# Optimization experiments

Hardware: AMD Instinct MI355X
Metric: run time of the kernel (lower is better)

Reference implementation:

```python
import jax, jax.numpy as jnp
import numpy as np
from jax import lax

B, T = 32, 20
H, E, A, V = 256, 512, 256, 10000
GH, GW, D = 32, 32, 256          # info spatial grid and channel dim
P = GH * GW                      # num_pixels = 1024
IN_FLAT = P * D                  # 262144
REL = 128 * 128                  # 16384
LSTM_IN = E + D + H              # input to gate linears (x = [word, att_feat], then cat h)


def setup_inputs() -> dict:
    key = jax.random.key(0)
    ks = iter(jax.random.split(key, 40))
    def W(shape, scale=0.05):
        return jax.random.normal(next(ks), shape, jnp.float32) * scale
    inp = {}
    inp["info"] = jax.random.normal(next(ks), (B, GH, GW, D), jnp.float32)
    inp["relation"] = jax.random.normal(next(ks), (B, 128, 128), jnp.float32)
    inp["captions"] = jax.random.randint(next(ks), (B, T), 0, V)
    lens = jax.random.randint(next(ks), (B, 1), 5, T + 1).at[0, 0].set(T)
    inp["captions_lens"] = lens
    # embedding + attention
    inp["emb"] = W((V, E), 0.1)
    inp["W_enc"] = W((D, A)); inp["b_enc"] = jnp.zeros((A,), jnp.float32)
    inp["W_dec"] = W((H, A)); inp["b_dec"] = jnp.zeros((A,), jnp.float32)
    inp["W_full"] = W((A,));  inp["b_full"] = jnp.zeros((), jnp.float32)
    # MSLSTM cell (5 gate linears + mlp)
    for g in ("i", "f", "o", "g1", "g2"):
        inp[f"W_{g}"] = W((LSTM_IN, H)); inp[f"b_{g}"] = jnp.zeros((H,), jnp.float32)
    inp["W_mlp"] = W((2 * H, H)); inp["b_mlp"] = jnp.zeros((H,), jnp.float32)
    # f_beta, fc, init-state linears
    inp["W_beta"] = W((H, D)); inp["b_beta"] = jnp.zeros((D,), jnp.float32)
    inp["W_fc"] = W((H, V), 0.1); inp["b_fc"] = jnp.zeros((V,), jnp.float32)
    inp["W_ih"] = W((IN_FLAT, H), 0.005); inp["b_ih"] = jnp.zeros((H,), jnp.float32)
    inp["W_ic"] = W((IN_FLAT, H), 0.005); inp["b_ic"] = jnp.zeros((H,), jnp.float32)
    inp["W_iC"] = W((REL, H), 0.01);      inp["b_iC"] = jnp.zeros((H,), jnp.float32)
    return inp


def reference(info, relation, captions, captions_lens, emb,
              W_enc, b_enc, W_dec, b_dec, W_full, b_full,
              W_i, b_i, W_f, b_f, W_o, b_o, W_g1, b_g1, W_g2, b_g2,
              W_mlp, b_mlp, W_beta, b_beta, W_fc, b_fc,
              W_ih, b_ih, W_ic, b_ic, W_iC, b_iC):
    Bsz = captions.shape[0]
    info_f = info.reshape(Bsz, P, D)
    rel_f = relation.reshape(Bsz, REL)
    lens = captions_lens[:, 0]
    order = jnp.argsort(-lens)                      # sort descending by length
    lens = lens[order]
    caps = captions[order]
    info_f = info_f[order]
    rel_f = rel_f[order]
    sent_len = lens - 1
    Tm = captions.shape[1] - 1                      # static: max len forced to T in setup

    words = emb[caps]                               # (B, T, E)
    flat = info_f.reshape(Bsz, -1)                  # (B, P*D)
    h = flat @ W_ih + b_ih
    c = flat @ W_ic + b_ic
    C = rel_f @ W_iC + b_iC
    att1 = info_f @ W_enc + b_enc                   # (B, P, A) -- invariant over t

    def step(carry, xs):
        h, c, C = carry
        word, t = xs                                # word: (B, E)
        att2 = h @ W_dec + b_dec                    # (B, A)
        e = jax.nn.relu(att1 + att2[:, None, :]) @ W_full + b_full   # (B, P)
        alpha = jax.nn.softmax(e, axis=1)
        awf = jnp.einsum('bpd,bp->bd', info_f, alpha)                # (B, D)
        # note: gate=sigmoid(f_beta(h)) is computed in torch but its product is unused
        x = jnp.concatenate([word, awf, h], axis=1)  # cat([x, h]) with x=[word, awf]
        i = jax.nn.sigmoid(x @ W_i + b_i)
        f = jax.nn.sigmoid(x @ W_f + b_f)
        o = jax.nn.sigmoid(x @ W_o + b_o)
        g1 = jnp.tanh(x @ W_g1 + b_g1)
        g2 = jnp.tanh(x @ W_g2 + b_g2)
        new_c = f * c + i * g1
        new_C = f * C + i * g2
        new_h = o * jnp.tanh(jnp.concatenate([new_c, new_C], axis=1) @ W_mlp + b_mlp)
        pred = new_h @ W_fc + b_fc                  # dropout in eval mode = identity
        mask = (sent_len > t)[:, None].astype(pred.dtype)
        return (new_h, new_c, new_C), (pred * mask, alpha * mask)

    words_t = jnp.swapaxes(words[:, :Tm], 0, 1)     # (Tm, B, E)
    (_, (preds, alphas)) = lax.scan(step, (h, c, C), (words_t, jnp.arange(Tm)))
    predictions = jnp.swapaxes(preds, 0, 1)         # (B, Tm, V)
    alphas = jnp.swapaxes(alphas, 0, 1)             # (B, Tm, P)
    return predictions, alphas, order
```

## Files before the change

### kernel.cpp

```cpp
#include <hip/hip_runtime.h>
#include <math.h>

#define Bz 32
#define Tz 20
#define TMz 19
#define Vz 10000
#define INFLAT 262144
#define RELSZ 16384
#define NBLK 512

#define WS_PH     0
#define WS_PC     4194304
#define WS_ATT1H  0
#define WS_INFOH  4194304
#define WS_EXPE   8388608
#define WS_ZSUM   8421376
#define WS_AWF    8421888
#define WS_GSP    8430080
#define WS_HST    8593920
#define WS_CST0   8602112
#define WS_CSTB0  8610304
#define WS_CST1   8618496
#define WS_CSTB1  8626688
#define WS_AT2P   8634880
#define WS_INTS   8700416
#define WS_PCHC   8701440

__device__ __forceinline__ float sigm(float x) { return 1.0f / (1.0f + expf(-x)); }

__device__ __forceinline__ unsigned short f2bf(float f) {
    unsigned int x = __float_as_uint(f);
    unsigned int r = (x + 0x7fffu + ((x >> 16) & 1u)) >> 16;
    return (unsigned short)r;
}
__device__ __forceinline__ float bfl(unsigned int u) { return __uint_as_float(u << 16); }
__device__ __forceinline__ float bfh(unsigned int u) { return __uint_as_float(u & 0xffff0000u); }

__device__ __forceinline__ float agload(const float* p) {
    return __hip_atomic_load(p, __ATOMIC_RELAXED, __HIP_MEMORY_SCOPE_AGENT);
}
__device__ __forceinline__ void agstore(float* p, float v) {
    __hip_atomic_store(p, v, __ATOMIC_RELAXED, __HIP_MEMORY_SCOPE_AGENT);
}
__device__ __forceinline__ int agloadi(const int* p) {
    return __hip_atomic_load(p, __ATOMIC_RELAXED, __HIP_MEMORY_SCOPE_AGENT);
}
__device__ __forceinline__ void agstorei(int* p, int v) {
    __hip_atomic_store(p, v, __ATOMIC_RELAXED, __HIP_MEMORY_SCOPE_AGENT);
}
__device__ __forceinline__ void agadd(float* p, float v) {
    __hip_atomic_fetch_add(p, v, __ATOMIC_RELAXED, __HIP_MEMORY_SCOPE_AGENT);
}

__device__ __forceinline__ void gl_lds16(const float* g, float* l) {
    __builtin_amdgcn_global_load_lds(
        (const __attribute__((address_space(1))) unsigned int*)g,
        (__attribute__((address_space(3))) unsigned int*)l,
        16, 0, 0);
}

__device__ __forceinline__ void gbar(int* slots, int* root, int gen) {
    asm volatile("s_waitcnt vmcnt(0)" ::: "memory");
    __syncthreads();
    if (blockIdx.x == 0) {
        int i0 = threadIdx.x, i1 = threadIdx.x + 256;
        if (i0 != 0) {
            while (agloadi(&slots[i0]) < gen) __builtin_amdgcn_s_sleep(1);
        }
        while (agloadi(&slots[i1]) < gen) __builtin_amdgcn_s_sleep(1);
        __syncthreads();
        if (threadIdx.x == 0) agstorei(root, gen);
    } else if (threadIdx.x == 0) {
        agstorei(&slots[blockIdx.x], gen);
        while (agloadi(root) < gen) __builtin_amdgcn_s_sleep(2);
    }
    __syncthreads();
    asm volatile("" ::: "memory");
}

__global__ void k_sort(const int* __restrict__ lens, float* __restrict__ out_order,
                       int* __restrict__ ord, int* __restrict__ sentlen, int* __restrict__ barmem) {
    if (threadIdx.x == 0 && blockIdx.x == 0) {
        for (int i = 0; i < 64 + NBLK; ++i) barmem[i] = 0;
        int l[Bz]; bool used[Bz];
        for (int b = 0; b < Bz; ++b) { l[b] = lens[b]; used[b] = false; }
        for (int i = 0; i < Bz; ++i) {
            int best = -1;
            for (int j = 0; j < Bz; ++j)
                if (!used[j] && (best < 0 || l[j] > l[best])) best = j;
            used[best] = true;
            ord[i] = best;
            sentlen[i] = l[best] - 1;
            out_order[i] = (float)best;
        }
    }
}

__global__ __launch_bounds__(256) void k_gemv2(const float* __restrict__ X, const int* __restrict__ ord,
                                               const float* __restrict__ W1, const float* __restrict__ W2,
                                               float* __restrict__ p1, float* __restrict__ p2) {
    __shared__ __align__(16) float wlds[8192];
    __shared__ __align__(16) float xsT[256 * 36];
    __shared__ int ords[32];
    int tid = threadIdx.x;
    int wv = tid >> 6, ln = tid & 63;
    size_t k0 = (size_t)blockIdx.x * 512;

    if (tid < 32) ords[tid] = ord[tid];
    __syncthreads();

    auto stage_xs = [&](int hh) {
        for (int idx = tid; idx < 2048; idx += 256) {
            int b = idx >> 6, kq = idx & 63;
            float4 v = *(const float4*)&X[(size_t)ords[b] * INFLAT + k0 + (size_t)hh * 256 + kq * 4];
            xsT[(kq * 4 + 0) * 36 + b] = v.x;
            xsT[(kq * 4 + 1) * 36 + b] = v.y;
            xsT[(kq * 4 + 2) * 36 + b] = v.z;
            xsT[(kq * 4 + 3) * 36 + b] = v.w;
        }
    };
    auto issue = [&](int n) {
        int slot = n & 1;
        size_t krow = k0 + (size_t)n * 8 + wv * 2;
        const float* g1 = W1 + krow * 256 + ln * 4;
        const float* g2 = W2 + krow * 256 + ln * 4;
        float* l1 = &wlds[slot * 4096 + (wv * 2) * 256 + ln * 4];
        float* l2 = &wlds[slot * 4096 + 2048 + (wv * 2) * 256 + ln * 4];
        gl_lds16(g1, l1);
        gl_lds16(g2, l2);
        gl_lds16(g1 + 256, l1 + 256);
        gl_lds16(g2 + 256, l2 + 256);
    };

    float ah[32], ac[32];
#pragma unroll
    for (int b = 0; b < 32; ++b) { ah[b] = 0.f; ac[b] = 0.f; }

    stage_xs(0);
    issue(0);

#pragma unroll 1
    for (int c = 0; c < 64; ++c) {
        if (c == 32) stage_xs(1);
        if (c + 1 < 64) {
            issue(c + 1);
            asm volatile("s_waitcnt vmcnt(4)" ::: "memory");
        } else {
            asm volatile("s_waitcnt vmcnt(0)" ::: "memory");
        }
        __syncthreads();
        int slot = c & 1;
        int xb0 = (c & 31) * 8;
#pragma unroll
        for (int kk = 0; kk < 8; ++kk) {
            float w1 = wlds[slot * 4096 + kk * 256 + tid];
            float w2 = wlds[slot * 4096 + 2048 + kk * 256 + tid];
            const float4* xr = (const float4*)&xsT[(xb0 + kk) * 36];
#pragma unroll
            for (int bq = 0; bq < 8; ++bq) {
                float4 x4 = xr[bq];
                ah[bq * 4 + 0] += x4.x * w1; ac[bq * 4 + 0] += x4.x * w2;
                ah[bq * 4 + 1] += x4.y * w1; ac[bq * 4 + 1] += x4.y * w2;
                ah[bq * 4 + 2] += x4.z * w1; ac[bq * 4 + 2] += x4.z * w2;
                ah[bq * 4 + 3] += x4.w * w1; ac[bq * 4 + 3] += x4.w * w2;
            }
        }
        __syncthreads();
    }
#pragma unroll
    for (int b = 0; b < 32; ++b) {
        size_t o = ((size_t)blockIdx.x * 32 + b) * 256 + tid;
        p1[o] = ah[b];
        p2[o] = ac[b];
    }
}

__global__ __launch_bounds__(256) void k_gemvC(const float* __restrict__ R, const int* __restrict__ ord,
                                               const float* __restrict__ W, float* __restrict__ p) {
    __shared__ float xs[32 * 128];
    __shared__ int ords[32];
    int tid = threadIdx.x, bx = blockIdx.x;
    if (tid < 32) ords[tid] = ord[tid];
    __syncthreads();
    int k0 = bx * 128;
    for (int idx = tid; idx < 32 * 128; idx += 256) {
        int b = idx >> 7, kk = idx & 127;
        xs[idx] = R[(size_t)ords[b] * RELSZ + k0 + kk];
    }
    __syncthreads();
    float acc[32];
#pragma unroll
    for (int b = 0; b < 32; ++b) acc[b] = 0.f;
    for (int kk = 0; kk < 128; ++kk) {
        float w = W[(size_t)(k0 + kk) * 256 + tid];
#pragma unroll
        for (int b = 0; b < 32; ++b) acc[b] += xs[b * 128 + kk] * w;
    }
#pragma unroll
    for (int b = 0; b < 32; ++b) p[((size_t)bx * 32 + b) * 256 + tid] = acc[b];
}

__global__ __launch_bounds__(256) void k_reduce3(const float* __restrict__ ph, const float* __restrict__ pc,
                                                 const float* __restrict__ pC,
                                                 const float* __restrict__ b_ih, const float* __restrict__ b_ic,
                                                 const float* __restrict__ b_iC,
                                                 float* __restrict__ hst, float* __restrict__ cst,
                                                 float* __restrict__ Cst) {
    int which = blockIdx.x >> 5, b = blockIdx.x & 31, j = threadIdx.x;
    if (which == 0) {
        float s0 = b_ih[j], s1 = 0.f, s2 = 0.f, s3 = 0.f;
        for (int c = 0; c < 512; c += 4) {
            s0 += ph[((size_t)((c + 0) * 32 + b)) * 256 + j];
            s1 += ph[((size_t)((c + 1) * 32 + b)) * 256 + j];
            s2 += ph[((size_t)((c + 2) * 32 + b)) * 256 + j];
            s3 += ph[((size_t)((c + 3) * 32 + b)) * 256 + j];
        }
        hst[b * 256 + j] = s0 + s1 + s2 + s3;
    } else if (which == 1) {
        float s0 = b_ic[j], s1 = 0.f, s2 = 0.f, s3 = 0.f;
        for (int c = 0; c < 512; c += 4) {
            s0 += pc[((size_t)((c + 0) * 32 + b)) * 256 + j];
            s1 += pc[((size_t)((c + 1) * 32 + b)) * 256 + j];
            s2 += pc[((size_t)((c + 2) * 32 + b)) * 256 + j];
            s3 += pc[((size_t)((c + 3) * 32 + b)) * 256 + j];
        }
        cst[b * 256 + j] = s0 + s1 + s2 + s3;
    } else {
        float s0 = b_iC[j], s1 = 0.f, s2 = 0.f, s3 = 0.f;
        for (int c = 0; c < 128; c += 4) {
            s0 += pC[((size_t)((c + 0) * 32 + b)) * 256 + j];
            s1 += pC[((size_t)((c + 1) * 32 + b)) * 256 + j];
            s2 += pC[((size_t)((c + 2) * 32 + b)) * 256 + j];
            s3 += pC[((size_t)((c + 3) * 32 + b)) * 256 + j];
        }
        Cst[b * 256 + j] = s0 + s1 + s2 + s3;
    }
}

__global__ __launch_bounds__(256) void k_init2(const float* __restrict__ hst, const float* __restrict__ W_dec,
                                               float* __restrict__ at2p, float* __restrict__ awf,
                                               float* __restrict__ zsum) {
    __shared__ __align__(16) float hs[8192];
    int tid = threadIdx.x;
    for (int i = blockIdx.x * 256 + tid; i < 8192; i += 1024) awf[i] = 0.f;
    if (blockIdx.x == 0 && tid < 32) zsum[tid] = 0.f;
    for (int i = tid; i < 2048; i += 256) ((float4*)hs)[i] = ((const float4*)hst)[i];
    __syncthreads();
    int col = blockIdx.x * 64 + (tid & 63), bg = tid >> 6;
    float acc[8] = {0.f,0.f,0.f,0.f,0.f,0.f,0.f,0.f};
    for (int k = 0; k < 256; ++k) {
        float w = W_dec[(size_t)k * 256 + col];
#pragma unroll
        for (int bi = 0; bi < 8; ++bi) acc[bi] += hs[(bg * 8 + bi) * 256 + k] * w;
    }
#pragma unroll
    for (int bi = 0; bi < 8; ++bi) {
        int b = bg * 8 + bi;
        at2p[((size_t)(b * 8 + 0)) * 256 + col] = acc[bi];
#pragma unroll
        for (int ct = 1; ct < 8; ++ct) at2p[((size_t)(b * 8 + ct)) * 256 + col] = 0.f;
    }
}

__global__ __launch_bounds__(256) void k_att1(const float* __restrict__ info, const int* __restrict__ ord,
                                              const float* __restrict__ W, const float* __restrict__ bias,
                                              unsigned short* __restrict__ att1h,
                                              unsigned short* __restrict__ infoh) {
    __shared__ __align__(16) float xsT[256 * 36];
    int tid = threadIdx.x;
    int r0 = blockIdx.x * 32;
    int b = r0 >> 10, p0 = r0 & 1023;
    const float* src = info + (size_t)ord[b] * INFLAT + (size_t)p0 * 256;
    for (int idx = tid; idx < 2048; idx += 256) {
        int r = idx >> 6, kq = idx & 63;
        float4 v = *(const float4*)&src[r * 256 + kq * 4];
        xsT[(kq * 4 + 0) * 36 + r] = v.x;
        xsT[(kq * 4 + 1) * 36 + r] = v.y;
        xsT[(kq * 4 + 2) * 36 + r] = v.z;
        xsT[(kq * 4 + 3) * 36 + r] = v.w;
    }
    __syncthreads();
#pragma unroll 4
    for (int r = 0; r < 32; ++r)
        infoh[(size_t)(r0 + r) * 256 + tid] = f2bf(xsT[tid * 36 + r]);
    float acc[32];
#pragma unroll
    for (int r = 0; r < 32; ++r) acc[r] = 0.f;
    for (int k = 0; k < 256; ++k) {
        float w = W[k * 256 + tid];
        const float4* xr = (const float4*)&xsT[k * 36];
#pragma unroll
        for (int rq = 0; rq < 8; ++rq) {
            float4 x4 = xr[rq];
            acc[rq * 4 + 0] += x4.x * w;
            acc[rq * 4 + 1] += x4.y * w;
            acc[rq * 4 + 2] += x4.z * w;
            acc[rq * 4 + 3] += x4.w * w;
        }
    }
    float bj = bias[tid];
#pragma unroll
    for (int r = 0; r < 32; ++r)
        att1h[(size_t)(r0 + r) * 256 + tid] = f2bf(acc[r] + bj);
}

struct KArgs {
    const float *info, *emb, *W_dec, *b_dec, *W_full, *b_full;
    const float *W_i, *W_f, *W_o, *W_g1, *W_g2;
    const float *b_i, *b_f, *b_o, *b_g1, *b_g2;
    const float *W_mlp, *b_mlp, *W_fc, *b_fc;
    const int *caps;
    const unsigned short *att1h, *infoh;
    float *expe, *zsum, *awf, *gsp, *hst, *cst0, *Cst0, *cst1, *Cst1, *at2p;
    const int *ord, *slp;
    int *root, *slots;
    float *out_pred, *out_alpha;
};

__device__ void pred_task2(const KArgs& a, unsigned short* hb, int tile, int tm1) {
    int tid = threadIdx.x;
    for (int i = tid; i < 8192; i += 256) hb[i] = f2bf(agload(&a.hst[i]));
    __syncthreads();
    int col = tile * 64 + (tid & 63), bg = tid >> 6;
    if (col >= Vz) return;
    float acc[8] = {0.f, 0.f, 0.f, 0.f, 0.f, 0.f, 0.f, 0.f};
    for (int jq = 0; jq < 64; ++jq) {
        float w0 = a.W_fc[(size_t)(jq * 4 + 0) * Vz + col];
        float w1 = a.W_fc[(size_t)(jq * 4 + 1) * Vz + col];
        float w2 = a.W_fc[(size_t)(jq * 4 + 2) * Vz + col];
        float w3 = a.W_fc[(size_t)(jq * 4 + 3) * Vz + col];
#pragma unroll
        for (int bi = 0; bi < 8; ++bi) {
            uint2 u = *(const uint2*)&hb[(bg * 8 + bi) * 256 + jq * 4];
            acc[bi] += bfl(u.x) * w0 + bfh(u.x) * w1 + bfl(u.y) * w2 + bfh(u.y) * w3;
        }
    }
    float bv = a.b_fc[col];
#pragma unroll
    for (int bi = 0; bi < 8; ++bi) {
        int b = bg * 8 + bi;
        float r = (a.slp[b] > tm1) ? (acc[bi] + bv) : 0.f;
        a.out_pred[((size_t)b * TMz + tm1) * Vz + col] = r;
    }
}

__global__ __launch_bounds__(256, 2) void k_steps(KArgs a) {
    __shared__ __align__(16) unsigned char smem[81920];
    unsigned char* attB = smem;
    unsigned char* infB = smem + 32768;
    float* F = (float*)(smem + 65536);
    unsigned short* S16 = (unsigned short*)(smem + 65536);

    int bid = blockIdx.x, tid = threadIdx.x;
    int b = bid >> 4, sub = bid & 15;
    int gen = 0;

    {
        const unsigned short* ag = a.att1h + (size_t)(b * 1024 + sub * 64) * 256;
        const unsigned short* ig = a.infoh + (size_t)(b * 1024 + sub * 64) * 256;
        for (int idx = tid; idx < 2048; idx += 256) {
            int r = idx >> 5, qc = idx & 31;
            uint4 v = *(const uint4*)(ag + (size_t)r * 256 + qc * 8);
            *(uint4*)(attB + r * 512 + ((qc ^ (r & 7)) << 4)) = v;
            uint4 w2 = *(const uint4*)(ig + (size_t)r * 256 + qc * 8);
            *(uint4*)(infB + idx * 16) = w2;
        }
    }
    __syncthreads();

    for (int t = 0; t < TMz; ++t) {
        {
            float v = a.b_dec[tid];
#pragma unroll
            for (int ct = 0; ct < 8; ++ct) v += agload(&a.at2p[((size_t)(b * 8 + ct)) * 256 + tid]);
            F[tid] = v;
            F[256 + tid] = a.W_full[tid];
            __syncthreads();
            int pl = tid & 63, kq = tid >> 6;
            float part = 0.f;
#pragma unroll
            for (int q = 0; q < 8; ++q) {
                int c = kq * 8 + q;
                uint4 u = *(const uint4*)(attB + pl * 512 + ((c ^ (pl & 7)) << 4));
                const float* A = F + kq * 64 + q * 8;
                const float* W = F + 256 + kq * 64 + q * 8;
                part += fmaxf(bfl(u.x) + A[0], 0.f) * W[0];
                part += fmaxf(bfh(u.x) + A[1], 0.f) * W[1];
                part += fmaxf(bfl(u.y) + A[2], 0.f) * W[2];
                part += fmaxf(bfh(u.y) + A[3], 0.f) * W[3];
                part += fmaxf(bfl(u.z) + A[4], 0.f) * W[4];
                part += fmaxf(bfh(u.z) + A[5], 0.f) * W[5];
                part += fmaxf(bfl(u.w) + A[6], 0.f) * W[6];
                part += fmaxf(bfh(u.w) + A[7], 0.f) * W[7];
            }
            F[512 + kq * 64 + pl] = part;
            __syncthreads();
            if (tid < 64) {
                float e = F[512 + tid] + F[576 + tid] + F[640 + tid] + F[704 + tid] + a.b_full[0];
                float ex = expf(e);
                agstore(&a.expe[b * 1024 + sub * 64 + tid], ex);
                F[768 + tid] = ex;
                float s = ex;
                s += __shfl_down(s, 32); s += __shfl_down(s, 16); s += __shfl_down(s, 8);
                s += __shfl_down(s, 4);  s += __shfl_down(s, 2);  s += __shfl_down(s, 1);
                if (tid == 0) agadd(&a.zsum[b], s);
            }
            __syncthreads();
            int gg = tid >> 7, c2 = tid & 127;
            const unsigned char* ib = infB + gg * 512 + c2 * 4;
            const float* ex = F + 768;
            float a0 = 0.f, a1 = 0.f;
#pragma unroll
            for (int i = 0; i < 32; ++i) {
                unsigned int u = *(const unsigned int*)(ib + i * 1024);
                float ev = ex[i * 2 + gg];
                a0 += ev * bfl(u);
                a1 += ev * bfh(u);
            }
            F[832 + gg * 256 + c2 * 2]     = a0;
            F[832 + gg * 256 + c2 * 2 + 1] = a1;
            __syncthreads();
            agadd(&a.awf[b * 256 + tid], F[832 + tid] + F[1088 + tid]);
        }
        gbar(a.slots, a.root, ++gen);

        if (bid < 80) {
            int g = bid / 16, s16 = bid % 16;
            int ct = s16 >> 2, kc = s16 & 3;
            const float* Wg = (g == 0) ? a.W_i : (g == 1) ? a.W_f : (g == 2) ? a.W_o : (g == 3) ? a.W_g1 : a.W_g2;
            for (int idx = tid; idx < 8192; idx += 256) {
                int b2 = idx >> 8, kk = idx & 255;
                float v;
                if (kc == 0) {
                    int cap = a.caps[a.ord[b2] * Tz + t];
                    v = a.emb[(size_t)cap * 512 + kk];
                } else if (kc == 1) {
                    int cap = a.caps[a.ord[b2] * Tz + t];
                    v = a.emb[(size_t)cap * 512 + 256 + kk];
                } else if (kc == 2) {
                    v = agload(&a.awf[b2 * 256 + kk]);
                } else {
                    v = agload(&a.hst[b2 * 256 + kk]);
                }
                S16[idx] = f2bf(v);
            }
            __syncthreads();
            int col = ct * 64 + (tid & 63), bg = tid >> 6;
            float acc[8] = {0.f,0.f,0.f,0.f,0.f,0.f,0.f,0.f};
            int wbase = kc * 256;
            for (int kk = 0; kk < 256; kk += 4) {
                float w0 = Wg[(size_t)(wbase + kk + 0) * 256 + col];
                float w1 = Wg[(size_t)(wbase + kk + 1) * 256 + col];
                float w2 = Wg[(size_t)(wbase + kk + 2) * 256 + col];
                float w3 = Wg[(size_t)(wbase + kk + 3) * 256 + col];
#pragma unroll
                for (int bi = 0; bi < 8; ++bi) {
                    uint2 u = *(const uint2*)&S16[(bg * 8 + bi) * 256 + kk];
                    acc[bi] += bfl(u.x) * w0 + bfh(u.x) * w1 + bfl(u.y) * w2 + bfh(u.y) * w3;
                }
            }
            if (kc == 2) {
#pragma unroll
                for (int bi = 0; bi < 8; ++bi) {
                    float Z = agload(&a.zsum[bg * 8 + bi]);
                    acc[bi] *= (1.0f / Z);
                }
            }
#pragma unroll
            for (int bi = 0; bi < 8; ++bi)
                agstore(&a.gsp[((size_t)((g * 4 + kc) * 32 + bg * 8 + bi)) * 256 + col], acc[bi]);
        } else if (bid < 237) {
            if (bid < 112) {
                int bb = bid - 80;
                float Z = agload(&a.zsum[bb]);
                float invZ = 1.0f / Z;
                float am = (a.slp[bb] > t) ? invZ : 0.f;
                float* oal = a.out_alpha + ((size_t)bb * TMz + t) * 1024;
                for (int p = tid; p < 1024; p += 256) oal[p] = agload(&a.expe[bb * 1024 + p]) * am;
            }
            if (t > 0) pred_task2(a, S16, bid - 80, t - 1);
        }
        gbar(a.slots, a.root, ++gen);

        if (bid < 256) {
            int bb = bid >> 3, ct = bid & 7;
            int j = tid;
            const float* csOld = (t & 1) ? a.cst1 : a.cst0;
            const float* CsOld = (t & 1) ? a.Cst1 : a.Cst0;
            float* csNew = (t & 1) ? a.cst0 : a.cst1;
            float* CsNew = (t & 1) ? a.Cst0 : a.Cst1;
            float gs[5];
#pragma unroll
            for (int g = 0; g < 5; ++g) {
                float s = 0.f;
#pragma unroll
                for (int kc = 0; kc < 4; ++kc)
                    s += agload(&a.gsp[((size_t)((g * 4 + kc) * 32 + bb)) * 256 + j]);
                gs[g] = s;
            }
            gs[0] += a.b_i[j]; gs[1] += a.b_f[j]; gs[2] += a.b_o[j];
            gs[3] += a.b_g1[j]; gs[4] += a.b_g2[j];
            float iv = sigm(gs[0]), fv = sigm(gs[1]), ov = sigm(gs[2]);
            float g1 = tanhf(gs[3]), g2 = tanhf(gs[4]);
            float nc = fv * agload(&csOld[bb * 256 + j]) + iv * g1;
            float nC = fv * agload(&CsOld[bb * 256 + j]) + iv * g2;
            if (ct == 0) {
                agstore(&csNew[bb * 256 + j], nc);
                agstore(&CsNew[bb * 256 + j], nC);
            }
            if (ct == 1 && tid == 0) agstore(&a.zsum[bb], 0.f);
            F[j] = nc;
            F[256 + j] = nC;
            F[512 + j] = ov;
            __syncthreads();
            int colL = tid & 31, kth = tid >> 5;
            int col = ct * 32 + colL;
            float part = 0.f;
            const float* wm = a.W_mlp + col;
            for (int i = 0; i < 64; ++i) {
                int k = kth * 64 + i;
                part += F[k] * wm[(size_t)k * 256];
            }
            F[768 + colL * 9 + kth] = part;
            __syncthreads();
            if (tid < 32) {
                int c2 = ct * 32 + tid;
                float m = a.b_mlp[c2];
#pragma unroll
                for (int kk = 0; kk < 8; ++kk) m += F[768 + tid * 9 + kk];
                float hv = F[512 + c2] * tanhf(m);
                agstore(&a.hst[bb * 256 + c2], hv);
                F[1056 + tid] = hv;
                agstore(&a.awf[bb * 256 + c2], 0.f);
            }
            __syncthreads();
            float acc = 0.f;
            const float* wd = a.W_dec + (size_t)(ct * 32) * 256 + tid;
#pragma unroll
            for (int kk = 0; kk < 32; ++kk) acc += F[1056 + kk] * wd[(size_t)kk * 256];
            agstore(&a.at2p[((size_t)(bb * 8 + ct)) * 256 + tid], acc);
        }
        gbar(a.slots, a.root, ++gen);
    }

    if (bid >= 80 && bid < 237) pred_task2(a, S16, bid - 80, TMz - 1);
}

extern "C" void kernel_launch(void* const* d_in, const int* in_sizes, int n_in,
                              void* d_out, int out_size, void* d_ws, size_t ws_size,
                              hipStream_t stream) {
    const float* info  = (const float*)d_in[0];
    const float* rel   = (const float*)d_in[1];
    const int*   caps  = (const int*)d_in[2];
    const int*   lens  = (const int*)d_in[3];
    const float* emb   = (const float*)d_in[4];
    const float* W_enc = (const float*)d_in[5];
    const float* b_enc = (const float*)d_in[6];
    const float* W_dec = (const float*)d_in[7];
    const float* b_dec = (const float*)d_in[8];
    const float* W_full= (const float*)d_in[9];
    const float* b_full= (const float*)d_in[10];
    const float* W_i   = (const float*)d_in[11];
    const float* b_i   = (const float*)d_in[12];
    const float* W_f   = (const float*)d_in[13];
    const float* b_f   = (const float*)d_in[14];
    const float* W_o   = (const float*)d_in[15];
    const float* b_o   = (const float*)d_in[16];
    const float* W_g1  = (const float*)d_in[17];
    const float* b_g1  = (const float*)d_in[18];
    const float* W_g2  = (const float*)d_in[19];
    const float* b_g2  = (const float*)d_in[20];
    const float* W_mlp = (const float*)d_in[21];
    const float* b_mlp = (const float*)d_in[22];
    const float* W_fc  = (const float*)d_in[25];
    const float* b_fc  = (const float*)d_in[26];
    const float* W_ih  = (const float*)d_in[27];
    const float* b_ih  = (const float*)d_in[28];
    const float* W_ic  = (const float*)d_in[29];
    const float* b_ic  = (const float*)d_in[30];
    const float* W_iC  = (const float*)d_in[31];
    const float* b_iC  = (const float*)d_in[32];

    float* out = (float*)d_out;
    float* out_pred  = out;
    float* out_alpha = out + (size_t)Bz * TMz * Vz;
    float* out_order = out_alpha + (size_t)Bz * TMz * 1024;

    float* w = (float*)d_ws;
    float* ph   = w + WS_PH;
    float* pcp  = w + WS_PC;
    unsigned short* att1h = (unsigned short*)(w + WS_ATT1H);
    unsigned short* infoh = (unsigned short*)(w + WS_INFOH);
    float* expe = w + WS_EXPE;
    float* zsum = w + WS_ZSUM;
    float* awf  = w + WS_AWF;
    float* gsp  = w + WS_GSP;
    float* hst  = w + WS_HST;
    float* cst0 = w + WS_CST0;
    float* Cst0 = w + WS_CSTB0;
    float* cst1 = w + WS_CST1;
    float* Cst1 = w + WS_CSTB1;
    float* at2p = w + WS_AT2P;
    int*   ordp = (int*)(w + WS_INTS);
    int*   slp  = ordp + 32;
    int*   barmem = ordp + 64;
    float* pC   = w + WS_PCHC;

    k_sort<<<1, 64, 0, stream>>>(lens, out_order, ordp, slp, barmem);
    k_gemv2<<<512, 256, 0, stream>>>(info, ordp, W_ih, W_ic, ph, pcp);
    k_gemvC<<<128, 256, 0, stream>>>(rel, ordp, W_iC, pC);
    k_reduce3<<<96, 256, 0, stream>>>(ph, pcp, pC, b_ih, b_ic, b_iC, hst, cst0, Cst0);
    k_init2<<<4, 256, 0, stream>>>(hst, W_dec, at2p, awf, zsum);
    k_att1<<<1024, 256, 0, stream>>>(info, ordp, W_enc, b_enc, att1h, infoh);

    KArgs ka;
    ka.info = info; ka.emb = emb; ka.W_dec = W_dec; ka.b_dec = b_dec;
    ka.W_full = W_full; ka.b_full = b_full;
    ka.W_i = W_i; ka.W_f = W_f; ka.W_o = W_o; ka.W_g1 = W_g1; ka.W_g2 = W_g2;
    ka.b_i = b_i; ka.b_f = b_f; ka.b_o = b_o; ka.b_g1 = b_g1; ka.b_g2 = b_g2;
    ka.W_mlp = W_mlp; ka.b_mlp = b_mlp; ka.W_fc = W_fc; ka.b_fc = b_fc;
    ka.caps = caps;
    ka.att1h = att1h; ka.infoh = infoh;
    ka.expe = expe; ka.zsum = zsum; ka.awf = awf;
    ka.gsp = gsp; ka.hst = hst;
    ka.cst0 = cst0; ka.Cst0 = Cst0; ka.cst1 = cst1; ka.Cst1 = Cst1;
    ka.at2p = at2p;
    ka.ord = ordp; ka.slp = slp;
    ka.root = barmem; ka.slots = barmem + 64;
    ka.out_pred = out_pred; ka.out_alpha = out_alpha;

    k_steps<<<NBLK, 256, 0, stream>>>(ka);
}
```

Measured before the change: 2.184 ms.

## Pre-transpose gate and fc weights to column-major bf16 for step kernel

Adds two prologue kernels that convert the five LSTM gate weight matrices and W_fc into transposed bf16 copies in the workspace. Each column's weights become contiguous, so the persistent step kernel can load eight weights per 16-byte read, and the per-step weight traffic is halved. The conversion runs on every call and costs one extra pass over the weights. Rounding the weights to bf16 adds precision error, and each thread now reads along its own column with a large stride between neighbouring threads, which may hurt coalescing.

```diff
diff --git a/kernel.cpp b/kernel.cpp
--- a/kernel.cpp
+++ b/kernel.cpp
@@ -25,6 +25,9 @@
 #define WS_AT2P   8634880
 #define WS_INTS   8700416
 #define WS_PCHC   8701440
+#define WS_WG16   8701440
+#define WS_WFC16  9750016
+#define WS_END_WFC (9750016 + 1280000)
 
 __device__ __forceinline__ float sigm(float x) { return 1.0f / (1.0f + expf(-x)); }
 
@@ -260,6 +263,42 @@
 #pragma unroll
         for (int ct = 1; ct < 8; ++ct) at2p[((size_t)(b * 8 + ct)) * 256 + col] = 0.f;
     }
+}
+
+__global__ __launch_bounds__(256) void k_wfc16(const float* __restrict__ W_fc,
+                                               unsigned short* __restrict__ wfcT16) {
+    __shared__ unsigned short tile[16 * 256];
+    int tid = threadIdx.x;
+    int c0 = blockIdx.x * 16;
+    for (int p = 0; p < 16; ++p) {
+        int r = p * 16 + (tid >> 4);
+        int c = tid & 15;
+        tile[c * 256 + r] = f2bf(W_fc[(size_t)r * Vz + c0 + c]);
+    }
+    __syncthreads();
+    unsigned int* dst = (unsigned int*)wfcT16 + (size_t)c0 * 128;
+    const unsigned int* src = (const unsigned int*)tile;
+    for (int i = tid; i < 2048; i += 256) dst[i] = src[i];
+}
+
+__global__ __launch_bounds__(256) void k_wg16(const float* __restrict__ W_i, const float* __restrict__ W_f,
+                                              const float* __restrict__ W_o, const float* __restrict__ W_g1,
+                                              const float* __restrict__ W_g2,
+                                              unsigned short* __restrict__ wg16) {
+    __shared__ unsigned short tile[16 * 1024];
+    int tid = threadIdx.x;
+    int g = blockIdx.x >> 4;
+    int c0 = (blockIdx.x & 15) * 16;
+    const float* Wg = (g == 0) ? W_i : (g == 1) ? W_f : (g == 2) ? W_o : (g == 3) ? W_g1 : W_g2;
+    for (int p = 0; p < 64; ++p) {
+        int r = p * 16 + (tid >> 4);
+        int c = tid & 15;
+        tile[c * 1024 + r] = f2bf(Wg[(size_t)r * 256 + c0 + c]);
+    }
+    __syncthreads();
+    unsigned int* dst = (unsigned int*)wg16 + ((size_t)(g * 256 + c0)) * 512;
+    const unsigned int* src = (const unsigned int*)tile;
+    for (int i = tid; i < 8192; i += 256) dst[i] = src[i];
 }
 
 __global__ __launch_bounds__(256) void k_att1(const float* __restrict__ info, const int* __restrict__ ord,
@@ -306,11 +345,10 @@
 
 struct KArgs {
     const float *info, *emb, *W_dec, *b_dec, *W_full, *b_full;
-    const float *W_i, *W_f, *W_o, *W_g1, *W_g2;
     const float *b_i, *b_f, *b_o, *b_g1, *b_g2;
     const float *W_mlp, *b_mlp, *W_fc, *b_fc;
     const int *caps;
-    const unsigned short *att1h, *infoh;
+    const unsigned short *att1h, *infoh, *wfcT16, *wg16;
     float *expe, *zsum, *awf, *gsp, *hst, *cst0, *Cst0, *cst1, *Cst1, *at2p;
     const int *ord, *slp;
     int *root, *slots;
@@ -324,15 +362,31 @@
     int col = tile * 64 + (tid & 63), bg = tid >> 6;
     if (col >= Vz) return;
     float acc[8] = {0.f, 0.f, 0.f, 0.f, 0.f, 0.f, 0.f, 0.f};
-    for (int jq = 0; jq < 64; ++jq) {
-        float w0 = a.W_fc[(size_t)(jq * 4 + 0) * Vz + col];
-        float w1 = a.W_fc[(size_t)(jq * 4 + 1) * Vz + col];
-        float w2 = a.W_fc[(size_t)(jq * 4 + 2) * Vz + col];
-        float w3 = a.W_fc[(size_t)(jq * 4 + 3) * Vz + col];
-#pragma unroll
-        for (int bi = 0; bi < 8; ++bi) {
-            uint2 u = *(const uint2*)&hb[(bg * 8 + bi) * 256 + jq * 4];
-            acc[bi] += bfl(u.x) * w0 + bfh(u.x) * w1 + bfl(u.y) * w2 + bfh(u.y) * w3;
+    if (a.wfcT16) {
+        const uint4* wcol = (const uint4*)(a.wfcT16 + (size_t)col * 256);
+#pragma unroll 4
+        for (int q = 0; q < 32; ++q) {
+            uint4 u = wcol[q];
+            float w0 = bfl(u.x), w1 = bfh(u.x), w2 = bfl(u.y), w3 = bfh(u.y);
+            float w4 = bfl(u.z), w5 = bfh(u.z), w6 = bfl(u.w), w7 = bfh(u.w);
+#pragma unroll
+            for (int bi = 0; bi < 8; ++bi) {
+                uint4 hv = *(const uint4*)&hb[(bg * 8 + bi) * 256 + q * 8];
+                acc[bi] += bfl(hv.x) * w0 + bfh(hv.x) * w1 + bfl(hv.y) * w2 + bfh(hv.y) * w3
+                         + bfl(hv.z) * w4 + bfh(hv.z) * w5 + bfl(hv.w) * w6 + bfh(hv.w) * w7;
+            }
+        }
+    } else {
+        for (int jq = 0; jq < 64; ++jq) {
+            float w0 = a.W_fc[(size_t)(jq * 4 + 0) * Vz + col];
+            float w1 = a.W_fc[(size_t)(jq * 4 + 1) * Vz + col];
+            float w2 = a.W_fc[(size_t)(jq * 4 + 2) * Vz + col];
+            float w3 = a.W_fc[(size_t)(jq * 4 + 3) * Vz + col];
+#pragma unroll
+            for (int bi = 0; bi < 8; ++bi) {
+                uint2 u = *(const uint2*)&hb[(bg * 8 + bi) * 256 + jq * 4];
+                acc[bi] += bfl(u.x) * w0 + bfh(u.x) * w1 + bfl(u.y) * w2 + bfh(u.y) * w3;
+            }
         }
     }
     float bv = a.b_fc[col];
@@ -427,7 +481,6 @@
         if (bid < 80) {
             int g = bid / 16, s16 = bid % 16;
             int ct = s16 >> 2, kc = s16 & 3;
-            const float* Wg = (g == 0) ? a.W_i : (g == 1) ? a.W_f : (g == 2) ? a.W_o : (g == 3) ? a.W_g1 : a.W_g2;
             for (int idx = tid; idx < 8192; idx += 256) {
                 int b2 = idx >> 8, kk = idx & 255;
                 float v;
@@ -446,17 +499,18 @@
             }
             __syncthreads();
             int col = ct * 64 + (tid & 63), bg = tid >> 6;
+            const uint4* wcol = (const uint4*)(a.wg16 + ((size_t)(g * 256 + col)) * 1024 + kc * 256);
             float acc[8] = {0.f,0.f,0.f,0.f,0.f,0.f,0.f,0.f};
-            int wbase = kc * 256;
-            for (int kk = 0; kk < 256; kk += 4) {
-                float w0 = Wg[(size_t)(wbase + kk + 0) * 256 + col];
-                float w1 = Wg[(size_t)(wbase + kk + 1) * 256 + col];
-                float w2 = Wg[(size_t)(wbase + kk + 2) * 256 + col];
-                float w3 = Wg[(size_t)(wbase + kk + 3) * 256 + col];
+#pragma unroll 4
+            for (int q = 0; q < 32; ++q) {
+                uint4 u = wcol[q];
+                float w0 = bfl(u.x), w1 = bfh(u.x), w2 = bfl(u.y), w3 = bfh(u.y);
+                float w4 = bfl(u.z), w5 = bfh(u.z), w6 = bfl(u.w), w7 = bfh(u.w);
 #pragma unroll
                 for (int bi = 0; bi < 8; ++bi) {
-                    uint2 u = *(const uint2*)&S16[(bg * 8 + bi) * 256 + kk];
-                    acc[bi] += bfl(u.x) * w0 + bfh(u.x) * w1 + bfl(u.y) * w2 + bfh(u.y) * w3;
+                    uint4 xv = *(const uint4*)&S16[(bg * 8 + bi) * 256 + q * 8];
+                    acc[bi] += bfl(xv.x) * w0 + bfh(xv.x) * w1 + bfl(xv.y) * w2 + bfh(xv.y) * w3
+                             + bfl(xv.z) * w4 + bfh(xv.z) * w5 + bfl(xv.w) * w6 + bfh(xv.w) * w7;
                 }
             }
             if (kc == 2) {
@@ -605,22 +659,29 @@
     int*   slp  = ordp + 32;
     int*   barmem = ordp + 64;
     float* pC   = w + WS_PCHC;
+    unsigned short* wg16   = (unsigned short*)(w + WS_WG16);
+    unsigned short* wfcT16 = (unsigned short*)(w + WS_WFC16);
+
+    int useWfc = (ws_size >= (size_t)WS_END_WFC * 4);
 
     k_sort<<<1, 64, 0, stream>>>(lens, out_order, ordp, slp, barmem);
     k_gemv2<<<512, 256, 0, stream>>>(info, ordp, W_ih, W_ic, ph, pcp);
     k_gemvC<<<128, 256, 0, stream>>>(rel, ordp, W_iC, pC);
     k_reduce3<<<96, 256, 0, stream>>>(ph, pcp, pC, b_ih, b_ic, b_iC, hst, cst0, Cst0);
     k_init2<<<4, 256, 0, stream>>>(hst, W_dec, at2p, awf, zsum);
+    k_wg16<<<80, 256, 0, stream>>>(W_i, W_f, W_o, W_g1, W_g2, wg16);
+    if (useWfc) k_wfc16<<<625, 256, 0, stream>>>(W_fc, wfcT16);
     k_att1<<<1024, 256, 0, stream>>>(info, ordp, W_enc, b_enc, att1h, infoh);
 
     KArgs ka;
     ka.info = info; ka.emb = emb; ka.W_dec = W_dec; ka.b_dec = b_dec;
     ka.W_full = W_full; ka.b_full = b_full;
-    ka.W_i = W_i; ka.W_f = W_f; ka.W_o = W_o; ka.W_g1 = W_g1; ka.W_g2 = W_g2;
     ka.b_i = b_i; ka.b_f = b_f; ka.b_o = b_o; ka.b_g1 = b_g1; ka.b_g2 = b_g2;
     ka.W_mlp = W_mlp; ka.b_mlp = b_mlp; ka.W_fc = W_fc; ka.b_fc = b_fc;
     ka.caps = caps;
     ka.att1h = att1h; ka.infoh = infoh;
+    ka.wfcT16 = useWfc ? wfcT16 : (const unsigned short*)0;
+    ka.wg16 = wg16;
     ka.expe = expe; ka.zsum = zsum; ka.awf = awf;
     ka.gsp = gsp; ka.hst = hst;
     ka.cst0 = cst0; ka.Cst0 = Cst0; ka.cst1 = cst1; ka.Cst1 = Cst1;
```

Result: faster. 2.040 ms (-6.6%).
